# Kernel optimization log

Hardware: AMD Instinct MI355X
Metric: run time of the kernel (lower is better)

Reference implementation:

```python
import jax, jax.numpy as jnp
import numpy as np

N, D_IN, FC_DIM, GROUP, NONGT, EMB = 4096, 12544, 1024, 16, 300, 64
DG = FC_DIM // GROUP  # 64 per-head dim


def extract_position_matrix(bbox, nongt_dim):
    xmin, ymin, xmax, ymax = jnp.split(bbox, 4, axis=1)  # each [N,1]
    bw = xmax - xmin + 1.0
    bh = ymax - ymin + 1.0
    cx = 0.5 * (xmin + xmax)
    cy = 0.5 * (ymin + ymax)
    dx = jnp.log(jnp.maximum(jnp.abs((cx - cx.T) / bw), 1e-3))
    dy = jnp.log(jnp.maximum(jnp.abs((cy - cy.T) / bh), 1e-3))
    dw = jnp.log(bw / bw.T)
    dh = jnp.log(bh / bh.T)
    # slice to first nongt_dim columns, stack -> [N, nongt, 4]
    return jnp.stack([dx[:, :nongt_dim], dy[:, :nongt_dim],
                      dw[:, :nongt_dim], dh[:, :nongt_dim]], axis=2)


def extract_position_embedding(pos_mat, feat_dim=64, wave_length=1000.0):
    n8 = feat_dim // 8
    feat_range = jnp.arange(n8, dtype=pos_mat.dtype)
    dim_mat = wave_length ** (8.0 / feat_dim * feat_range)  # [8]
    div = 100.0 * pos_mat[..., None] / dim_mat              # [N,nongt,4,8]
    emb = jnp.concatenate([jnp.sin(div), jnp.cos(div)], axis=3)  # [N,nongt,4,16]
    return emb.reshape(pos_mat.shape[0], pos_mat.shape[1], feat_dim)


def attention_multi_head(feat, pos_emb, Wpos, bpos, Wq, bq, Wk, bk, Wo, bo):
    # feat: [N, 1024], pos_emb: [N, nongt, 64]
    nongt_feat = feat[:NONGT]                                   # [nongt, 1024]
    aff_w = jax.nn.relu(pos_emb @ Wpos + bpos)                  # [N, nongt, G]
    aff_w = jnp.swapaxes(aff_w, 1, 2)                           # [N, G, nongt]
    q = (feat @ Wq + bq).reshape(-1, GROUP, DG)                 # [N, G, dg]
    k = (nongt_feat @ Wk + bk).reshape(NONGT, GROUP, DG)        # [nongt, G, dg]
    aff = jnp.einsum('ngd,mgd->ngm', q, k) * (1.0 / np.sqrt(DG))  # [N, G, nongt]
    logits = jnp.log(jnp.maximum(aff_w, 1e-6)) + aff
    p = jax.nn.softmax(logits, axis=2)                          # [N, G, nongt]
    out = jnp.einsum('ngm,mc->ngc', p, nongt_feat)              # [N, G, 1024]
    # grouped 1x1 conv: group g maps 1024 -> 64 outputs
    lin = jnp.einsum('ngc,goc->ngo', out, Wo) + bo.reshape(GROUP, DG)
    return lin.reshape(feat.shape[0], FC_DIM)


def setup_inputs() -> dict:
    key = jax.random.key(0)
    ks = jax.random.split(key, 20)
    roi_feat = jax.random.normal(ks[0], (N, D_IN), dtype=jnp.float32)
    u = jax.random.uniform(ks[1], (N, 4), dtype=jnp.float32)
    x1 = u[:, 0:1] * 500.0
    y1 = u[:, 1:2] * 500.0
    bbox = jnp.concatenate([x1, y1, x1 + u[:, 2:3] * 200.0 + 1.0,
                            y1 + u[:, 3:4] * 200.0 + 1.0], axis=1)
    def lin(k, fin, fout):
        s = 1.0 / np.sqrt(fin)
        return jax.random.normal(k, (fin, fout), dtype=jnp.float32) * s
    inp = {'roi_feat': roi_feat, 'bbox': bbox,
           'W_fc1': lin(ks[2], D_IN, FC_DIM), 'b_fc1': jnp.zeros((FC_DIM,), jnp.float32),
           'W_fc2': lin(ks[3], FC_DIM, FC_DIM), 'b_fc2': jnp.zeros((FC_DIM,), jnp.float32)}
    for i, base in [(1, 4), (2, 10)]:
        inp[f'Wpos{i}'] = lin(ks[base], EMB, GROUP)
        inp[f'bpos{i}'] = jnp.zeros((GROUP,), jnp.float32)
        inp[f'Wq{i}'] = lin(ks[base + 1], FC_DIM, FC_DIM)
        inp[f'bq{i}'] = jnp.zeros((FC_DIM,), jnp.float32)
        inp[f'Wk{i}'] = lin(ks[base + 2], FC_DIM, FC_DIM)
        inp[f'bk{i}'] = jnp.zeros((FC_DIM,), jnp.float32)
        inp[f'Wo{i}'] = jax.random.normal(ks[base + 3], (GROUP, DG, FC_DIM), dtype=jnp.float32) * (1.0 / np.sqrt(FC_DIM))
        inp[f'bo{i}'] = jnp.zeros((FC_DIM,), jnp.float32)
    return inp


def reference(roi_feat, bbox, W_fc1, b_fc1, W_fc2, b_fc2,
              Wpos1, bpos1, Wq1, bq1, Wk1, bk1, Wo1, bo1,
              Wpos2, bpos2, Wq2, bq2, Wk2, bk2, Wo2, bo2):
    pos_mat = extract_position_matrix(bbox, NONGT)
    pos_emb = extract_position_embedding(pos_mat, EMB)
    x = roi_feat
    for (Wf, bf, Wp, bp, Wq, bq, Wk, bk, Wo, bo) in [
        (W_fc1, b_fc1, Wpos1, bpos1, Wq1, bq1, Wk1, bk1, Wo1, bo1),
        (W_fc2, b_fc2, Wpos2, bpos2, Wq2, bq2, Wk2, bk2, Wo2, bo2)]:
        x = x @ Wf + bf
        attn = attention_multi_head(x, pos_emb, Wp, bp, Wq, bq, Wk, bk, Wo, bo)
        x = jax.nn.relu(x + attn)
    return x
```

## Files before the change

kernel.cpp:

```cpp
#include <hip/hip_runtime.h>


using bf16x8 = __attribute__((ext_vector_type(8))) short;
using u16x4  = __attribute__((ext_vector_type(4))) short;
using f32x4  = __attribute__((ext_vector_type(4))) float;
typedef unsigned short u16;
typedef unsigned int   u32;

#define DEV __device__ __forceinline__

DEV u32 cvtpk(float lo, float hi) {
  u32 r;
  asm("v_cvt_pk_bf16_f32 %0, %1, %2" : "=v"(r) : "v"(lo), "v"(hi));
  return r;
}
DEV u16 f2bf(float f) { return (u16)cvtpk(f, f); }
DEV float bf2f(u16 h) { return __uint_as_float(((u32)h) << 16); }

DEV f32x4 mfma16(bf16x8 a, bf16x8 b, f32x4 c) {
  return __builtin_amdgcn_mfma_f32_16x16x32_bf16(a, b, c, 0, 0, 0);
}
DEV void gload16(const u16* g, u16* l) {
  __builtin_amdgcn_global_load_lds((const __attribute__((address_space(1))) void*)g,
                                   (__attribute__((address_space(3))) void*)l, 16, 0, 0);
}

DEV void fsincos(float x, float* s, float* c) {
  float r = x * 0.15915494309189535f;
  r -= rintf(r);
  float a = r * 6.283185307179586f;
  *s = __sinf(a); *c = __cosf(a);
}

struct PrepArgs {
  const float* Wo1; u16* Wo1_b;
  const float* Wo2; u16* Wo2_b;
  const float* Wfc1; u16* Wfc1_t;
  const float* wsrc[5]; u16* wdst[5];
};

__global__ __launch_bounds__(256) void prep_kernel(PrepArgs p) {
  __shared__ float tp[32][36];
  int b = blockIdx.x, tid = threadIdx.x;
  if (b < 1024) {
    const float* src = (b < 512) ? p.Wo1 : p.Wo2;
    u16* dst = (b < 512) ? p.Wo1_b : p.Wo2_b;
    size_t i = ((size_t)(b & 511) * 256 + tid) * 8;
    float4 a = *(const float4*)(src + i);
    float4 c = *(const float4*)(src + i + 4);
    int4 v;
    v.x = (int)cvtpk(a.x, a.y); v.y = (int)cvtpk(a.z, a.w);
    v.z = (int)cvtpk(c.x, c.y); v.w = (int)cvtpk(c.z, c.w);
    *(int4*)(dst + i) = v;
    return;
  }
  const float* in; u16* out; int r0, c0, R, C;
  if (b < 13568) {
    int idx = b - 1024;
    in = p.Wfc1; out = p.Wfc1_t; R = 12544; C = 1024;
    r0 = (idx >> 5) * 32; c0 = (idx & 31) * 32;
  } else {
    int idx = b - 13568;
    int z = idx >> 10, rest = idx & 1023;
    in = p.wsrc[z]; out = p.wdst[z]; R = 1024; C = 1024;
    r0 = (rest >> 5) * 32; c0 = (rest & 31) * 32;
  }
  {
    int r = tid >> 3, c4 = (tid & 7) * 4;
    float4 v = *(const float4*)(in + (size_t)(r0 + r) * C + c0 + c4);
    *(float4*)&tp[r][c4] = v;
  }
  __syncthreads();
  {
    int c = tid >> 3, r4 = (tid & 7) * 4;
    u32 lo = cvtpk(tp[r4 + 0][c], tp[r4 + 1][c]);
    u32 hi = cvtpk(tp[r4 + 2][c], tp[r4 + 3][c]);
    int2 v; v.x = (int)lo; v.y = (int)hi;
    *(int2*)(out + (size_t)(c0 + c) * R + r0 + r4) = v;
  }
}

__global__ __launch_bounds__(512, 2) void gemm8p(
    const float* __restrict__ A, const u16* __restrict__ Bt,
    float* __restrict__ P) {
  const int K = 12544;
  __shared__ u16 lds[65536];
  int tid = threadIdx.x;
  int w = tid >> 6, l = tid & 63, h = l >> 4, l15 = l & 15;
  int wm = w >> 2, wn = w & 3;

  int b = ((blockIdx.x & 7) << 5) | (blockIdx.x >> 3);
  int bz = b >> 6, rest = b & 63;
  int bm = (rest & 15) * 256;
  int bn = (rest >> 4) * 256;
  size_t k0 = (size_t)bz * 3136;

  int arow = tid >> 3;
  int c0 = (tid & 7) * 8;
  const float* pA0 = A + (size_t)(bm + arow) * K + k0 + c0;
  const size_t aseg = (size_t)64 * K;
  int awe = ((arow * 128 + c0 * 2) ^ ((arow & 7) << 4)) >> 1;

  int X = ((tid >> 3) & 7) << 4;
  int lb2 = (tid * 16) ^ X;
  int lr = lb2 >> 7, lc = (lb2 & 127) >> 1;
  const u16* pB = Bt + (size_t)(bn + lr) * K + k0 + lc;
  const size_t o64 = (size_t)64 * K, o128 = (size_t)128 * K, o192 = (size_t)192 * K;

  int swz = (l15 & 7) << 3;
  int xk0 = (h * 8) ^ swz;
  int xk1 = 32 ^ xk0;
  int rA = (wm * 64 + l15) * 64;
  int rB = (wn * 32 + l15) * 64;

  f32x4 acc[8][4];
#pragma unroll
  for (int i = 0; i < 8; i++)
#pragma unroll
    for (int j = 0; j < 4; j++) acc[i][j] = (f32x4){0.f, 0.f, 0.f, 0.f};

  float4 a0[4], a1[4];
  bf16x8 af[4][2], bl[2][2], bh[2][2];

#define AISSUE(kk) { _Pragma("unroll") for (int s = 0; s < 4; s++) {     \
    a0[s] = *(const float4*)(pA0 + s * aseg + (kk));                     \
    a1[s] = *(const float4*)(pA0 + s * aseg + (kk) + 4); } }
#define BISSUE_LO(WB, kk) {                                              \
    gload16(pB + (kk),        (WB) + tid * 8);                           \
    gload16(pB + o64 + (kk),  (WB) + 4096 + tid * 8); }
#define BISSUE_HI(WB, kk) {                                              \
    gload16(pB + o128 + (kk), (WB) + 8192 + tid * 8);                    \
    gload16(pB + o192 + (kk), (WB) + 12288 + tid * 8); }
#define AWRITE(WA) { _Pragma("unroll") for (int s = 0; s < 4; s++) {     \
    int4 v;                                                              \
    v.x = (int)cvtpk(a0[s].x, a0[s].y);                                  \
    v.y = (int)cvtpk(a0[s].z, a0[s].w);                                  \
    v.z = (int)cvtpk(a1[s].x, a1[s].y);                                  \
    v.w = (int)cvtpk(a1[s].z, a1[s].w);                                  \
    *(int4*)&(WA)[awe + s * 4096] = v; } }
#define READ_AF(BASE)                                                    \
  _Pragma("unroll") for (int i = 0; i < 4; i++) {                        \
    af[i][0] = *(const bf16x8*)&LA[(BASE) + rA + i * 1024 + xk0];        \
    af[i][1] = *(const bf16x8*)&LA[(BASE) + rA + i * 1024 + xk1];        \
  }
#define READ_BL {                                                        \
  _Pragma("unroll") for (int j = 0; j < 2; j++) {                        \
    bl[j][0] = *(const bf16x8*)&LB[rB + j * 1024 + xk0];                 \
    bl[j][1] = *(const bf16x8*)&LB[rB + j * 1024 + xk1]; } }
#define READ_BH {                                                        \
  _Pragma("unroll") for (int j = 0; j < 2; j++) {                        \
    bh[j][0] = *(const bf16x8*)&LB[8192 + rB + j * 1024 + xk0];          \
    bh[j][1] = *(const bf16x8*)&LB[8192 + rB + j * 1024 + xk1]; } }
#define Q_MFMA(QR, QC, BF)                                               \
  __builtin_amdgcn_s_setprio(1);                                         \
  _Pragma("unroll") for (int i = 0; i < 4; i++)                          \
    _Pragma("unroll") for (int j = 0; j < 2; j++) {                      \
      acc[(QR)*4+i][(QC)*2+j] = mfma16(af[i][0], BF[j][0], acc[(QR)*4+i][(QC)*2+j]); \
      acc[(QR)*4+i][(QC)*2+j] = mfma16(af[i][1], BF[j][1], acc[(QR)*4+i][(QC)*2+j]); \
    }                                                                    \
  __builtin_amdgcn_s_setprio(0);
#define SBAR __builtin_amdgcn_sched_barrier(0)

  AISSUE(0);
  BISSUE_LO(lds + 16384, 0);
  BISSUE_HI(lds + 16384, 0);
  AWRITE(lds);
  asm volatile("s_waitcnt vmcnt(0) lgkmcnt(0)" ::: "memory");
  __builtin_amdgcn_s_barrier();

  for (int t = 0; t < 48; t++) {
    const u16* LA = lds + (t & 1) * 32768;
    const u16* LB = LA + 16384;
    u16* WA = lds + ((t + 1) & 1) * 32768;
    u16* WB = WA + 16384;
    int ktn = (t + 1) * 64;
    AISSUE(ktn);
    asm volatile("s_waitcnt vmcnt(10) lgkmcnt(0)" ::: "memory");
    __builtin_amdgcn_s_barrier();
    SBAR;
    READ_AF(0);
    READ_BL;
    Q_MFMA(0, 0, bl);
    SBAR;
    BISSUE_LO(WB, ktn);
    asm volatile("s_waitcnt vmcnt(10)" ::: "memory");
    __builtin_amdgcn_s_barrier();
    SBAR;
    READ_BH;
    Q_MFMA(0, 1, bh);
    SBAR;
    BISSUE_HI(WB, ktn);
    READ_AF(8192);
    Q_MFMA(1, 1, bh);
    SBAR;
    Q_MFMA(1, 0, bl);
    SBAR;
    AWRITE(WA);
  }
  {
    const u16* LA = lds;
    const u16* LB = lds + 16384;
    asm volatile("s_waitcnt vmcnt(2) lgkmcnt(0)" ::: "memory");
    __builtin_amdgcn_s_barrier();
    SBAR;
    READ_AF(0);
    READ_BL;
    Q_MFMA(0, 0, bl);
    SBAR;
    asm volatile("s_waitcnt vmcnt(0)" ::: "memory");
    __builtin_amdgcn_s_barrier();
    SBAR;
    READ_BH;
    Q_MFMA(0, 1, bh);
    SBAR;
    READ_AF(8192);
    Q_MFMA(1, 1, bh);
    Q_MFMA(1, 0, bl);
  }
#undef AISSUE
#undef BISSUE_LO
#undef BISSUE_HI
#undef AWRITE
#undef READ_AF
#undef READ_BL
#undef READ_BH
#undef Q_MFMA
#undef SBAR

  float* dst = P + (size_t)bz * 4096 * 1024;
#pragma unroll
  for (int qr = 0; qr < 2; qr++)
#pragma unroll
    for (int i = 0; i < 4; i++)
#pragma unroll
      for (int qc = 0; qc < 2; qc++)
#pragma unroll
        for (int j = 0; j < 2; j++) {
          int row0 = bm + qr * 128 + wm * 64 + i * 16 + h * 4;
          int col  = bn + qc * 128 + wn * 32 + j * 16 + l15;
          f32x4 v = acc[qr * 4 + i][qc * 2 + j];
#pragma unroll
          for (int r = 0; r < 4; r++)
            dst[(size_t)(row0 + r) * 1024 + col] = v[r];
        }
}

__constant__ float C100D[8] = {100.f, 42.16965034285822f, 17.78279410038923f,
                               7.498942093324559f, 3.1622776601683795f,
                               1.333521432163324f, 0.5623413251903491f,
                               0.23713737056616552f};

__global__ __launch_bounds__(256) void reduce_pos_kernel(
    const float* __restrict__ P, const float* __restrict__ bias,
    float* __restrict__ xf, u16* __restrict__ xb,
    const float* __restrict__ bbox,
    const float* __restrict__ Wpos1, const float* __restrict__ Wpos2,
    const float* __restrict__ bpos1, const float* __restrict__ bpos2,
    u16* __restrict__ logw1, u16* __restrict__ logw2) {
  __shared__ u16 pool[18944];
  int tid = threadIdx.x;
  if (blockIdx.x < 2048) {
    const size_t MN = (size_t)4096 * 1024;
    size_t i = ((size_t)blockIdx.x * 256 + tid) * 4;
    size_t stride = (size_t)2048 * 256 * 4;
    for (; i < MN; i += stride) {
      float4 a = *(const float4*)(P + i);
      float4 b = *(const float4*)(P + MN + i);
      float4 c = *(const float4*)(P + 2 * MN + i);
      float4 d = *(const float4*)(P + 3 * MN + i);
      float4 bv = *(const float4*)(bias + (i & 1023));
      float4 r;
      r.x = a.x + b.x + c.x + d.x + bv.x;
      r.y = a.y + b.y + c.y + d.y + bv.y;
      r.z = a.z + b.z + c.z + d.z + bv.z;
      r.w = a.w + b.w + c.w + d.w + bv.w;
      *(float4*)(xf + i) = r;
      int2 hv; hv.x = (int)cvtpk(r.x, r.y); hv.y = (int)cvtpk(r.z, r.w);
      *(int2*)(xb + i) = hv;
    }
    return;
  }
  u16* emb_s = pool;
  u16* wp_s  = pool + 5632;
  u16* lw_s  = pool + 8448;
  int n = blockIdx.x - 2048;
  int w = tid >> 6, l = tid & 63, h = l >> 4, l15 = l & 15;
  for (int idx = tid; idx < 1024; idx += 256) {
    int e = idx >> 4, c = idx & 15;
    wp_s[c * 88 + e]        = f2bf(Wpos1[idx]);
    wp_s[(16 + c) * 88 + e] = f2bf(Wpos2[idx]);
  }
  float4 bn = ((const float4*)bbox)[n];
  float bw_n = bn.z - bn.x + 1.f, bh_n = bn.w - bn.y + 1.f;
  float cx_n = 0.5f * (bn.x + bn.z), cy_n = 0.5f * (bn.y + bn.w);
  float bps0 = bpos1[l15], bps1 = bpos2[l15];
  int p = tid >> 2, k = tid & 3;

  for (int m0 = 0; m0 < 320; m0 += 64) {
    int m = m0 + p;
    float4 bm = ((const float4*)bbox)[m];
    float v;
    if (k == 0)      v = logf(fmaxf(fabsf((cx_n - 0.5f * (bm.x + bm.z)) / bw_n), 1e-3f));
    else if (k == 1) v = logf(fmaxf(fabsf((cy_n - 0.5f * (bm.y + bm.w)) / bh_n), 1e-3f));
    else if (k == 2) v = logf(bw_n / (bm.z - bm.x + 1.f));
    else             v = logf(bh_n / (bm.w - bm.y + 1.f));
    __syncthreads();
#pragma unroll
    for (int tt = 0; tt < 8; tt++) {
      float s, c; fsincos(v * C100D[tt], &s, &c);
      emb_s[p * 88 + k * 16 + tt]     = f2bf(s);
      emb_s[p * 88 + k * 16 + 8 + tt] = f2bf(c);
    }
    __syncthreads();
    f32x4 acc0 = {0.f, 0.f, 0.f, 0.f}, acc1 = {0.f, 0.f, 0.f, 0.f};
    bf16x8 a0 = *(const bf16x8*)&emb_s[(w * 16 + l15) * 88 + h * 8];
    bf16x8 a1 = *(const bf16x8*)&emb_s[(w * 16 + l15) * 88 + 32 + h * 8];
    bf16x8 b00 = *(const bf16x8*)&wp_s[l15 * 88 + h * 8];
    bf16x8 b01 = *(const bf16x8*)&wp_s[l15 * 88 + 32 + h * 8];
    bf16x8 b10 = *(const bf16x8*)&wp_s[(16 + l15) * 88 + h * 8];
    bf16x8 b11 = *(const bf16x8*)&wp_s[(16 + l15) * 88 + 32 + h * 8];
    acc0 = mfma16(a0, b00, acc0); acc0 = mfma16(a1, b01, acc0);
    acc1 = mfma16(a0, b10, acc1); acc1 = mfma16(a1, b11, acc1);
#pragma unroll
    for (int r = 0; r < 4; r++) {
      int mm = m0 + w * 16 + h * 4 + r;
      lw_s[l15 * 328 + mm]        = f2bf(logf(fmaxf(acc0[r] + bps0, 1e-6f)));
      lw_s[(16 + l15) * 328 + mm] = f2bf(logf(fmaxf(acc1[r] + bps1, 1e-6f)));
    }
  }
  __syncthreads();
  for (int i = tid; i < 1280; i += 256) {
    int layer = i / 640, rest = i - layer * 640;
    int gg = rest / 40, seg = rest - gg * 40;
    bf16x8 v = *(const bf16x8*)&lw_s[(layer * 16 + gg) * 328 + seg * 8];
    u16* dst = (layer ? logw2 : logw1) + ((size_t)gg * 4096 + n) * 320 + seg * 8;
    *(bf16x8*)dst = v;
  }
}

struct GDesc {
  const u16* A; const u16* Bt; const float* bias;
  u16* Cb; float* Cf;
  int M, N, K, ldc, nt;
};

__global__ __launch_bounds__(256, 2) void gemmU(GDesc g0, GDesc g1, GDesc g2,
                                                int c0, int c1) {
  __shared__ u16 lds[32768];
  GDesc g; int lb = blockIdx.x;
  if (lb < c0) { g = g0; lb = (lb & 7) * (c0 >> 3) + (lb >> 3); }
  else if (lb < c1) { g = g1; lb -= c0; }
  else { g = g2; lb -= c1; }
  int bm = (lb / g.nt) * 128, bn = (lb % g.nt) * 128;
  int tid = threadIdx.x;
  int w = tid >> 6, l = tid & 63, h = l >> 4, l15 = l & 15;
  int wm = w >> 1, wn = w & 1;
  int K = g.K;

  int X = ((tid >> 3) & 7) << 4;
  int lbyte = (tid * 16) ^ X;
  int lr = lbyte >> 7, lc = (lbyte & 127) >> 1;
  const u16 *pa[4], *pb[4];
#pragma unroll
  for (int c = 0; c < 4; c++) {
    pa[c] = g.A  + (size_t)min(bm + c * 32 + lr, g.M - 1) * K + lc;
    pb[c] = g.Bt + (size_t)min(bn + c * 32 + lr, g.N - 1) * K + lc;
  }

  int swz = (l15 & 7) << 3;
  int xk0 = (h * 8) ^ swz;
  int xk1 = 32 ^ xk0;
  int rA = (wm * 64 + l15) * 64;
  int rB = (wn * 64 + l15) * 64;

  f32x4 acc[4][4];
#pragma unroll
  for (int i = 0; i < 4; i++)
#pragma unroll
    for (int j = 0; j < 4; j++) acc[i][j] = (f32x4){0.f, 0.f, 0.f, 0.f};

#define ISSUEU(W, kk)                                     \
  { gload16(pa[0] + (kk), (W) + tid * 8);                 \
    gload16(pa[1] + (kk), (W) + 2048 + tid * 8);          \
    gload16(pa[2] + (kk), (W) + 4096 + tid * 8);          \
    gload16(pa[3] + (kk), (W) + 6144 + tid * 8);          \
    gload16(pb[0] + (kk), (W) + 8192 + tid * 8);          \
    gload16(pb[1] + (kk), (W) + 10240 + tid * 8);         \
    gload16(pb[2] + (kk), (W) + 12288 + tid * 8);         \
    gload16(pb[3] + (kk), (W) + 14336 + tid * 8); }

  ISSUEU(lds, 0);
  int ktiles = K >> 6;
  for (int t = 0; t < ktiles; t++) {
    const u16* LA = lds + (t & 1) * 16384;
    const u16* LB = LA + 8192;
    u16* W = lds + ((t ^ 1) & 1) * 16384;
    if (t < ktiles - 1) {
      ISSUEU(W, (t + 1) * 64);
      asm volatile("s_waitcnt vmcnt(8)" ::: "memory");
    } else {
      asm volatile("s_waitcnt vmcnt(0)" ::: "memory");
    }
    __builtin_amdgcn_s_barrier();
    asm volatile("" ::: "memory");
    bf16x8 a[4][2], bfr[4][2];
#pragma unroll
    for (int i = 0; i < 4; i++) {
      a[i][0] = *(const bf16x8*)&LA[rA + i * 1024 + xk0];
      a[i][1] = *(const bf16x8*)&LA[rA + i * 1024 + xk1];
    }
#pragma unroll
    for (int j = 0; j < 4; j++) {
      bfr[j][0] = *(const bf16x8*)&LB[rB + j * 1024 + xk0];
      bfr[j][1] = *(const bf16x8*)&LB[rB + j * 1024 + xk1];
    }
    __builtin_amdgcn_s_setprio(1);
#pragma unroll
    for (int i = 0; i < 4; i++)
#pragma unroll
      for (int j = 0; j < 4; j++) {
        acc[i][j] = mfma16(a[i][0], bfr[j][0], acc[i][j]);
        acc[i][j] = mfma16(a[i][1], bfr[j][1], acc[i][j]);
      }
    __builtin_amdgcn_s_setprio(0);
    asm volatile("" ::: "memory");
    __builtin_amdgcn_s_barrier();
  }
#undef ISSUEU

#pragma unroll
  for (int i = 0; i < 4; i++) {
#pragma unroll
    for (int j = 0; j < 4; j++) {
      int col = bn + wn * 64 + j * 16 + l15;
      if (col >= g.ldc) continue;
      float bv = (g.bias != nullptr && col < g.N) ? g.bias[col] : 0.f;
      int row0 = bm + wm * 64 + i * 16 + h * 4;
#pragma unroll
      for (int r = 0; r < 4; r++) {
        int row = row0 + r;
        if (row >= g.M) continue;
        float v = acc[i][j][r] + bv;
        size_t off = (size_t)row * g.ldc + col;
        g.Cb[off] = f2bf(v);
        if (g.Cf != nullptr) g.Cf[off] = v;
      }
    }
  }
}

template <bool LAST>
__global__ __launch_bounds__(256) void attn_kernel(
    const u16* __restrict__ qb, const u16* __restrict__ kb,
    const u16* __restrict__ kvt, const u16* __restrict__ logw,
    const float* __restrict__ xf, const float* __restrict__ bo,
    float* __restrict__ outf, u16* __restrict__ outb) {
  __shared__ u16 ps[64 * 344];
  int tid = threadIdx.x;
  int g = blockIdx.y, n0 = blockIdx.x * 64;
  int w = tid >> 6, l = tid & 63, h = l >> 4, l15 = l & 15;

  {
    const u16* src = logw + ((size_t)g * 4096 + n0) * 320;
    for (int i = tid; i < 64 * 40; i += 256) {
      int row = i / 40, seg = i - row * 40;
      *(bf16x8*)&ps[row * 328 + seg * 8] = *(const bf16x8*)(src + row * 320 + seg * 8);
    }
  }
  int nrow = n0 + w * 16 + l15;
  const u16* qp = qb + (size_t)nrow * 1024 + g * 64;
  bf16x8 aq0 = *(const bf16x8*)(qp + h * 8);
  bf16x8 aq1 = *(const bf16x8*)(qp + 32 + h * 8);

  f32x4 acc[19];
#pragma unroll
  for (int f = 0; f < 19; f++) acc[f] = (f32x4){0.f, 0.f, 0.f, 0.f};
  const u16* kp = kb + g * 64 + h * 8;
#pragma unroll
  for (int f = 0; f < 19; f++) {
    bf16x8 b0 = *(const bf16x8*)(kp + (size_t)(f * 16 + l15) * 1024);
    bf16x8 b1 = *(const bf16x8*)(kp + (size_t)(f * 16 + l15) * 1024 + 32);
    acc[f] = mfma16(aq0, b0, acc[f]);
    acc[f] = mfma16(aq1, b1, acc[f]);
  }
  __syncthreads();

  int nbase = n0 + w * 16 + h * 4;
  int lrow = w * 16 + h * 4;
  float mx[4] = {-INFINITY, -INFINITY, -INFINITY, -INFINITY};
  float sm[4] = {0.f, 0.f, 0.f, 0.f};
#pragma unroll
  for (int f = 0; f < 19; f++) {
    int m = f * 16 + l15;
#pragma unroll
    for (int r = 0; r < 4; r++) {
      float lw = -INFINITY;
      if (m < 300) lw = bf2f(ps[(lrow + r) * 328 + m]);
      float lg = acc[f][r] * 0.125f + lw;
      acc[f][r] = lg;
      mx[r] = fmaxf(mx[r], lg);
    }
  }
#pragma unroll
  for (int d = 1; d < 16; d <<= 1)
#pragma unroll
    for (int r = 0; r < 4; r++) mx[r] = fmaxf(mx[r], __shfl_xor(mx[r], d));
#pragma unroll
  for (int f = 0; f < 19; f++)
#pragma unroll
    for (int r = 0; r < 4; r++) {
      float p = __expf(acc[f][r] - mx[r]);
      acc[f][r] = p; sm[r] += p;
    }
#pragma unroll
  for (int d = 1; d < 16; d <<= 1)
#pragma unroll
    for (int r = 0; r < 4; r++) sm[r] += __shfl_xor(sm[r], d);
  float inv[4];
#pragma unroll
  for (int r = 0; r < 4; r++) inv[r] = 1.f / sm[r];

  __syncthreads();
#pragma unroll
  for (int f = 0; f < 19; f++)
#pragma unroll
    for (int r = 0; r < 4; r++)
      ps[(lrow + r) * 344 + f * 16 + l15] = f2bf(acc[f][r]);
#pragma unroll
  for (int r = 0; r < 4; r++)
    ps[(lrow + r) * 344 + 304 + l15] = 0;

  f32x4 acc2[4];
#pragma unroll
  for (int fo = 0; fo < 4; fo++) acc2[fo] = (f32x4){0.f, 0.f, 0.f, 0.f};
  const u16* vp = kvt + (size_t)g * 64 * 320 + h * 8;
#pragma unroll
  for (int ks = 0; ks < 10; ks++) {
    bf16x8 ap = *(const bf16x8*)&ps[(w * 16 + l15) * 344 + ks * 32 + h * 8];
#pragma unroll
    for (int fo = 0; fo < 4; fo++) {
      bf16x8 bv = *(const bf16x8*)(vp + (size_t)(fo * 16 + l15) * 320 + ks * 32);
      acc2[fo] = mfma16(ap, bv, acc2[fo]);
    }
  }
#pragma unroll
  for (int fo = 0; fo < 4; fo++) {
    int col = g * 64 + fo * 16 + l15;
    float bov = bo[col];
#pragma unroll
    for (int r = 0; r < 4; r++) {
      int row = nbase + r;
      float v = xf[(size_t)row * 1024 + col] + acc2[fo][r] * inv[r] + bov;
      v = fmaxf(v, 0.f);
      if (LAST) outf[(size_t)row * 1024 + col] = v;
      else      outb[(size_t)row * 1024 + col] = f2bf(v);
    }
  }
}

extern "C" void kernel_launch(void* const* d_in, const int* in_sizes, int n_in,
                              void* d_out, int out_size, void* d_ws, size_t ws_size,
                              hipStream_t stream) {
  (void)in_sizes; (void)n_in; (void)out_size; (void)ws_size;
  const float* roi   = (const float*)d_in[0];
  const float* bbox  = (const float*)d_in[1];
  const float* Wfc1  = (const float*)d_in[2];
  const float* bfc1  = (const float*)d_in[3];
  const float* Wfc2  = (const float*)d_in[4];
  const float* bfc2  = (const float*)d_in[5];
  const float* Wpos1 = (const float*)d_in[6];
  const float* bpos1 = (const float*)d_in[7];
  const float* Wq1   = (const float*)d_in[8];
  const float* bq1   = (const float*)d_in[9];
  const float* Wk1   = (const float*)d_in[10];
  const float* bk1   = (const float*)d_in[11];
  const float* Wo1   = (const float*)d_in[12];
  const float* bo1   = (const float*)d_in[13];
  const float* Wpos2 = (const float*)d_in[14];
  const float* bpos2 = (const float*)d_in[15];
  const float* Wq2   = (const float*)d_in[16];
  const float* bq2   = (const float*)d_in[17];
  const float* Wk2   = (const float*)d_in[18];
  const float* bk2   = (const float*)d_in[19];
  const float* Wo2   = (const float*)d_in[20];
  const float* bo2   = (const float*)d_in[21];

  char* ws = (char*)d_ws;
  u16*  Wfc1_t = (u16*)(ws + 102760448);
  u16*  Wfc2_t = (u16*)(ws + 128450560);
  u16*  Wq1_t  = (u16*)(ws + 130547712);
  u16*  Wk1_t  = (u16*)(ws + 132644864);
  u16*  Wq2_t  = (u16*)(ws + 134742016);
  u16*  Wk2_t  = (u16*)(ws + 136839168);
  u16*  Wo1_b  = (u16*)(ws + 138936320);
  u16*  Wo2_b  = (u16*)(ws + 141033472);
  float* Pp    = (float*)(ws + 143134720);
  float* xf    = (float*)(ws + 227020800);
  u16*  xb_f   = (u16*)(ws + 243798016);
  u16*  xb_a   = (u16*)(ws + 252186624);
  u16*  q_b    = (u16*)(ws + 260575232);
  u16*  k_b    = (u16*)(ws + 268963840);
  u16*  kvt_b  = (u16*)(ws + 269578240);
  u16*  logw1  = (u16*)(ws + 270233600);
  u16*  logw2  = (u16*)(ws + 312176640);

  {
    PrepArgs p;
    p.Wo1 = Wo1;   p.Wo1_b = Wo1_b;
    p.Wo2 = Wo2;   p.Wo2_b = Wo2_b;
    p.Wfc1 = Wfc1; p.Wfc1_t = Wfc1_t;
    p.wsrc[0] = Wfc2; p.wdst[0] = Wfc2_t;
    p.wsrc[1] = Wq1;  p.wdst[1] = Wq1_t;
    p.wsrc[2] = Wk1;  p.wdst[2] = Wk1_t;
    p.wsrc[3] = Wq2;  p.wdst[3] = Wq2_t;
    p.wsrc[4] = Wk2;  p.wdst[4] = Wk2_t;
    prep_kernel<<<18688, 256, 0, stream>>>(p);
  }
  gemm8p<<<256, 512, 0, stream>>>(roi, Wfc1_t, Pp);
  reduce_pos_kernel<<<6144, 256, 0, stream>>>(Pp, bfc1, xf, xb_f, bbox,
                                              Wpos1, Wpos2, bpos1, bpos2,
                                              logw1, logw2);
  {
    GDesc q  = {xb_f,  Wq1_t, bq1, q_b,   nullptr, 4096, 1024, 1024, 1024, 8};
    GDesc kk = {xb_f,  Wk1_t, bk1, k_b,   nullptr,  300, 1024, 1024, 1024, 8};
    GDesc kv = {Wo1_b, xb_f,  nullptr, kvt_b, nullptr, 1024, 300, 1024, 320, 3};
    gemmU<<<304, 256, 0, stream>>>(q, kk, kv, 256, 280);
  }
  attn_kernel<false><<<dim3(64, 16), 256, 0, stream>>>(q_b, k_b, kvt_b, logw1, xf, bo1, nullptr, xb_a);

  {
    GDesc fc = {xb_a, Wfc2_t, bfc2, xb_f, xf, 4096, 1024, 1024, 1024, 8};
    gemmU<<<256, 256, 0, stream>>>(fc, fc, fc, 256, 256);
  }
  {
    GDesc q  = {xb_f,  Wq2_t, bq2, q_b,   nullptr, 4096, 1024, 1024, 1024, 8};
    GDesc kk = {xb_f,  Wk2_t, bk2, k_b,   nullptr,  300, 1024, 1024, 1024, 8};
    GDesc kv = {Wo2_b, xb_f,  nullptr, kvt_b, nullptr, 1024, 300, 1024, 320, 3};
    gemmU<<<304, 256, 0, stream>>>(q, kk, kv, 256, 280);
  }
  attn_kernel<true><<<dim3(64, 16), 256, 0, stream>>>(q_b, k_b, kvt_b, logw2, xf, bo2, (float*)d_out, nullptr);
}
```

Baseline: 381.8 us.

## Move position-embedding work into prep kernel, drop fp32 residual copy, raise MFMA priority

The position-embedding and log-weight computation moves out of the post-GEMM reduce kernel and into the weight-prep kernel, so it no longer follows the big FC1 GEMM. The fp32 residual buffer xf is removed: the reduce and FC2 GEMM write only bf16, and the attention kernel reads the bf16 residual. This cuts fp32 write and read traffic. s_setprio is also placed around the MFMA loops in the attention kernel. The residual now carries bf16 rounding, which may reduce accuracy.

```diff
diff --git a/kernel.cpp b/kernel.cpp
--- a/kernel.cpp
+++ b/kernel.cpp
@@ -2,7 +2,6 @@
 
 
 using bf16x8 = __attribute__((ext_vector_type(8))) short;
-using u16x4  = __attribute__((ext_vector_type(4))) short;
 using f32x4  = __attribute__((ext_vector_type(4))) float;
 typedef unsigned short u16;
 typedef unsigned int   u32;
@@ -32,20 +31,89 @@
   *s = __sinf(a); *c = __cosf(a);
 }
 
-struct PrepArgs {
+__constant__ float C100D[8] = {100.f, 42.16965034285822f, 17.78279410038923f,
+                               7.498942093324559f, 3.1622776601683795f,
+                               1.333521432163324f, 0.5623413251903491f,
+                               0.23713737056616552f};
+
+struct PrepPosArgs {
+  const float* bbox;
+  const float* Wpos1; const float* Wpos2;
+  const float* bpos1; const float* bpos2;
+  u16* logw1; u16* logw2;
   const float* Wo1; u16* Wo1_b;
   const float* Wo2; u16* Wo2_b;
   const float* Wfc1; u16* Wfc1_t;
   const float* wsrc[5]; u16* wdst[5];
 };
 
-__global__ __launch_bounds__(256) void prep_kernel(PrepArgs p) {
-  __shared__ float tp[32][36];
+__global__ __launch_bounds__(256) void prep_pos_kernel(PrepPosArgs p) {
+  __shared__ u16 pool[18944];
   int b = blockIdx.x, tid = threadIdx.x;
-  if (b < 1024) {
-    const float* src = (b < 512) ? p.Wo1 : p.Wo2;
-    u16* dst = (b < 512) ? p.Wo1_b : p.Wo2_b;
-    size_t i = ((size_t)(b & 511) * 256 + tid) * 8;
+  if (b < 4096) {
+    u16* emb_s = pool;
+    u16* wp_s  = pool + 5632;
+    u16* lw_s  = pool + 8448;
+    int n = b;
+    int w = tid >> 6, l = tid & 63, h = l >> 4, l15 = l & 15;
+    for (int idx = tid; idx < 1024; idx += 256) {
+      int e = idx >> 4, c = idx & 15;
+      wp_s[c * 88 + e]        = f2bf(p.Wpos1[idx]);
+      wp_s[(16 + c) * 88 + e] = f2bf(p.Wpos2[idx]);
+    }
+    float4 bn = ((const float4*)p.bbox)[n];
+    float bw_n = bn.z - bn.x + 1.f, bh_n = bn.w - bn.y + 1.f;
+    float cx_n = 0.5f * (bn.x + bn.z), cy_n = 0.5f * (bn.y + bn.w);
+    float bps0 = p.bpos1[l15], bps1 = p.bpos2[l15];
+    int pr = tid >> 2, k = tid & 3;
+
+    for (int m0 = 0; m0 < 320; m0 += 64) {
+      int m = m0 + pr;
+      float4 bm = ((const float4*)p.bbox)[m];
+      float v;
+      if (k == 0)      v = logf(fmaxf(fabsf((cx_n - 0.5f * (bm.x + bm.z)) / bw_n), 1e-3f));
+      else if (k == 1) v = logf(fmaxf(fabsf((cy_n - 0.5f * (bm.y + bm.w)) / bh_n), 1e-3f));
+      else if (k == 2) v = logf(bw_n / (bm.z - bm.x + 1.f));
+      else             v = logf(bh_n / (bm.w - bm.y + 1.f));
+      __syncthreads();
+#pragma unroll
+      for (int tt = 0; tt < 8; tt++) {
+        float s, c; fsincos(v * C100D[tt], &s, &c);
+        emb_s[pr * 88 + k * 16 + tt]     = f2bf(s);
+        emb_s[pr * 88 + k * 16 + 8 + tt] = f2bf(c);
+      }
+      __syncthreads();
+      f32x4 acc0 = {0.f, 0.f, 0.f, 0.f}, acc1 = {0.f, 0.f, 0.f, 0.f};
+      bf16x8 a0 = *(const bf16x8*)&emb_s[(w * 16 + l15) * 88 + h * 8];
+      bf16x8 a1 = *(const bf16x8*)&emb_s[(w * 16 + l15) * 88 + 32 + h * 8];
+      bf16x8 b00 = *(const bf16x8*)&wp_s[l15 * 88 + h * 8];
+      bf16x8 b01 = *(const bf16x8*)&wp_s[l15 * 88 + 32 + h * 8];
+      bf16x8 b10 = *(const bf16x8*)&wp_s[(16 + l15) * 88 + h * 8];
+      bf16x8 b11 = *(const bf16x8*)&wp_s[(16 + l15) * 88 + 32 + h * 8];
+      acc0 = mfma16(a0, b00, acc0); acc0 = mfma16(a1, b01, acc0);
+      acc1 = mfma16(a0, b10, acc1); acc1 = mfma16(a1, b11, acc1);
+#pragma unroll
+      for (int r = 0; r < 4; r++) {
+        int mm = m0 + w * 16 + h * 4 + r;
+        lw_s[l15 * 328 + mm]        = f2bf(logf(fmaxf(acc0[r] + bps0, 1e-6f)));
+        lw_s[(16 + l15) * 328 + mm] = f2bf(logf(fmaxf(acc1[r] + bps1, 1e-6f)));
+      }
+    }
+    __syncthreads();
+    for (int i = tid; i < 1280; i += 256) {
+      int layer = i / 640, rest = i - layer * 640;
+      int gg = rest / 40, seg = rest - gg * 40;
+      bf16x8 v = *(const bf16x8*)&lw_s[(layer * 16 + gg) * 328 + seg * 8];
+      u16* dst = (layer ? p.logw2 : p.logw1) + ((size_t)gg * 4096 + n) * 320 + seg * 8;
+      *(bf16x8*)dst = v;
+    }
+    return;
+  }
+  int b2 = b - 4096;
+  if (b2 < 1024) {
+    const float* src = (b2 < 512) ? p.Wo1 : p.Wo2;
+    u16* dst = (b2 < 512) ? p.Wo1_b : p.Wo2_b;
+    size_t i = ((size_t)(b2 & 511) * 256 + tid) * 8;
     float4 a = *(const float4*)(src + i);
     float4 c = *(const float4*)(src + i + 4);
     int4 v;
@@ -54,13 +122,14 @@
     *(int4*)(dst + i) = v;
     return;
   }
+  float (*tp)[36] = (float(*)[36])pool;
   const float* in; u16* out; int r0, c0, R, C;
-  if (b < 13568) {
-    int idx = b - 1024;
+  if (b2 < 13568) {
+    int idx = b2 - 1024;
     in = p.Wfc1; out = p.Wfc1_t; R = 12544; C = 1024;
     r0 = (idx >> 5) * 32; c0 = (idx & 31) * 32;
   } else {
-    int idx = b - 13568;
+    int idx = b2 - 13568;
     int z = idx >> 10, rest = idx & 1023;
     in = p.wsrc[z]; out = p.wdst[z]; R = 1024; C = 1024;
     r0 = (rest >> 5) * 32; c0 = (rest & 31) * 32;
@@ -73,9 +142,9 @@
   __syncthreads();
   {
     int c = tid >> 3, r4 = (tid & 7) * 4;
-    u32 lo = cvtpk(tp[r4 + 0][c], tp[r4 + 1][c]);
-    u32 hi = cvtpk(tp[r4 + 2][c], tp[r4 + 3][c]);
-    int2 v; v.x = (int)lo; v.y = (int)hi;
+    int2 v;
+    v.x = (int)cvtpk(tp[r4 + 0][c], tp[r4 + 1][c]);
+    v.y = (int)cvtpk(tp[r4 + 2][c], tp[r4 + 3][c]);
     *(int2*)(out + (size_t)(c0 + c) * R + r0 + r4) = v;
   }
 }
@@ -245,102 +314,31 @@
         }
 }
 
-__constant__ float C100D[8] = {100.f, 42.16965034285822f, 17.78279410038923f,
-                               7.498942093324559f, 3.1622776601683795f,
-                               1.333521432163324f, 0.5623413251903491f,
-                               0.23713737056616552f};
-
-__global__ __launch_bounds__(256) void reduce_pos_kernel(
+__global__ __launch_bounds__(256) void reduce_kernel(
     const float* __restrict__ P, const float* __restrict__ bias,
-    float* __restrict__ xf, u16* __restrict__ xb,
-    const float* __restrict__ bbox,
-    const float* __restrict__ Wpos1, const float* __restrict__ Wpos2,
-    const float* __restrict__ bpos1, const float* __restrict__ bpos2,
-    u16* __restrict__ logw1, u16* __restrict__ logw2) {
-  __shared__ u16 pool[18944];
-  int tid = threadIdx.x;
-  if (blockIdx.x < 2048) {
-    const size_t MN = (size_t)4096 * 1024;
-    size_t i = ((size_t)blockIdx.x * 256 + tid) * 4;
-    size_t stride = (size_t)2048 * 256 * 4;
-    for (; i < MN; i += stride) {
-      float4 a = *(const float4*)(P + i);
-      float4 b = *(const float4*)(P + MN + i);
-      float4 c = *(const float4*)(P + 2 * MN + i);
-      float4 d = *(const float4*)(P + 3 * MN + i);
-      float4 bv = *(const float4*)(bias + (i & 1023));
-      float4 r;
-      r.x = a.x + b.x + c.x + d.x + bv.x;
-      r.y = a.y + b.y + c.y + d.y + bv.y;
-      r.z = a.z + b.z + c.z + d.z + bv.z;
-      r.w = a.w + b.w + c.w + d.w + bv.w;
-      *(float4*)(xf + i) = r;
-      int2 hv; hv.x = (int)cvtpk(r.x, r.y); hv.y = (int)cvtpk(r.z, r.w);
-      *(int2*)(xb + i) = hv;
-    }
-    return;
-  }
-  u16* emb_s = pool;
-  u16* wp_s  = pool + 5632;
-  u16* lw_s  = pool + 8448;
-  int n = blockIdx.x - 2048;
-  int w = tid >> 6, l = tid & 63, h = l >> 4, l15 = l & 15;
-  for (int idx = tid; idx < 1024; idx += 256) {
-    int e = idx >> 4, c = idx & 15;
-    wp_s[c * 88 + e]        = f2bf(Wpos1[idx]);
-    wp_s[(16 + c) * 88 + e] = f2bf(Wpos2[idx]);
-  }
-  float4 bn = ((const float4*)bbox)[n];
-  float bw_n = bn.z - bn.x + 1.f, bh_n = bn.w - bn.y + 1.f;
-  float cx_n = 0.5f * (bn.x + bn.z), cy_n = 0.5f * (bn.y + bn.w);
-  float bps0 = bpos1[l15], bps1 = bpos2[l15];
-  int p = tid >> 2, k = tid & 3;
-
-  for (int m0 = 0; m0 < 320; m0 += 64) {
-    int m = m0 + p;
-    float4 bm = ((const float4*)bbox)[m];
-    float v;
-    if (k == 0)      v = logf(fmaxf(fabsf((cx_n - 0.5f * (bm.x + bm.z)) / bw_n), 1e-3f));
-    else if (k == 1) v = logf(fmaxf(fabsf((cy_n - 0.5f * (bm.y + bm.w)) / bh_n), 1e-3f));
-    else if (k == 2) v = logf(bw_n / (bm.z - bm.x + 1.f));
-    else             v = logf(bh_n / (bm.w - bm.y + 1.f));
-    __syncthreads();
-#pragma unroll
-    for (int tt = 0; tt < 8; tt++) {
-      float s, c; fsincos(v * C100D[tt], &s, &c);
-      emb_s[p * 88 + k * 16 + tt]     = f2bf(s);
-      emb_s[p * 88 + k * 16 + 8 + tt] = f2bf(c);
-    }
-    __syncthreads();
-    f32x4 acc0 = {0.f, 0.f, 0.f, 0.f}, acc1 = {0.f, 0.f, 0.f, 0.f};
-    bf16x8 a0 = *(const bf16x8*)&emb_s[(w * 16 + l15) * 88 + h * 8];
-    bf16x8 a1 = *(const bf16x8*)&emb_s[(w * 16 + l15) * 88 + 32 + h * 8];
-    bf16x8 b00 = *(const bf16x8*)&wp_s[l15 * 88 + h * 8];
-    bf16x8 b01 = *(const bf16x8*)&wp_s[l15 * 88 + 32 + h * 8];
-    bf16x8 b10 = *(const bf16x8*)&wp_s[(16 + l15) * 88 + h * 8];
-    bf16x8 b11 = *(const bf16x8*)&wp_s[(16 + l15) * 88 + 32 + h * 8];
-    acc0 = mfma16(a0, b00, acc0); acc0 = mfma16(a1, b01, acc0);
-    acc1 = mfma16(a0, b10, acc1); acc1 = mfma16(a1, b11, acc1);
-#pragma unroll
-    for (int r = 0; r < 4; r++) {
-      int mm = m0 + w * 16 + h * 4 + r;
-      lw_s[l15 * 328 + mm]        = f2bf(logf(fmaxf(acc0[r] + bps0, 1e-6f)));
-      lw_s[(16 + l15) * 328 + mm] = f2bf(logf(fmaxf(acc1[r] + bps1, 1e-6f)));
-    }
-  }
-  __syncthreads();
-  for (int i = tid; i < 1280; i += 256) {
-    int layer = i / 640, rest = i - layer * 640;
-    int gg = rest / 40, seg = rest - gg * 40;
-    bf16x8 v = *(const bf16x8*)&lw_s[(layer * 16 + gg) * 328 + seg * 8];
-    u16* dst = (layer ? logw2 : logw1) + ((size_t)gg * 4096 + n) * 320 + seg * 8;
-    *(bf16x8*)dst = v;
+    u16* __restrict__ xb) {
+  const size_t MN = (size_t)4096 * 1024;
+  size_t i = ((size_t)blockIdx.x * 256 + threadIdx.x) * 4;
+  size_t stride = (size_t)2048 * 256 * 4;
+  for (; i < MN; i += stride) {
+    float4 a = *(const float4*)(P + i);
+    float4 b = *(const float4*)(P + MN + i);
+    float4 c = *(const float4*)(P + 2 * MN + i);
+    float4 d = *(const float4*)(P + 3 * MN + i);
+    float4 bv = *(const float4*)(bias + (i & 1023));
+    float4 r;
+    r.x = a.x + b.x + c.x + d.x + bv.x;
+    r.y = a.y + b.y + c.y + d.y + bv.y;
+    r.z = a.z + b.z + c.z + d.z + bv.z;
+    r.w = a.w + b.w + c.w + d.w + bv.w;
+    int2 hv; hv.x = (int)cvtpk(r.x, r.y); hv.y = (int)cvtpk(r.z, r.w);
+    *(int2*)(xb + i) = hv;
   }
 }
 
 struct GDesc {
   const u16* A; const u16* Bt; const float* bias;
-  u16* Cb; float* Cf;
+  u16* Cb;
   int M, N, K, ldc, nt;
 };
 
@@ -440,10 +438,7 @@
       for (int r = 0; r < 4; r++) {
         int row = row0 + r;
         if (row >= g.M) continue;
-        float v = acc[i][j][r] + bv;
-        size_t off = (size_t)row * g.ldc + col;
-        g.Cb[off] = f2bf(v);
-        if (g.Cf != nullptr) g.Cf[off] = v;
+        g.Cb[(size_t)row * g.ldc + col] = f2bf(acc[i][j][r] + bv);
       }
     }
   }
@@ -453,7 +448,7 @@
 __global__ __launch_bounds__(256) void attn_kernel(
     const u16* __restrict__ qb, const u16* __restrict__ kb,
     const u16* __restrict__ kvt, const u16* __restrict__ logw,
-    const float* __restrict__ xf, const float* __restrict__ bo,
+    const u16* __restrict__ xr, const float* __restrict__ bo,
     float* __restrict__ outf, u16* __restrict__ outb) {
   __shared__ u16 ps[64 * 344];
   int tid = threadIdx.x;
@@ -476,6 +471,7 @@
 #pragma unroll
   for (int f = 0; f < 19; f++) acc[f] = (f32x4){0.f, 0.f, 0.f, 0.f};
   const u16* kp = kb + g * 64 + h * 8;
+  __builtin_amdgcn_s_setprio(1);
 #pragma unroll
   for (int f = 0; f < 19; f++) {
     bf16x8 b0 = *(const bf16x8*)(kp + (size_t)(f * 16 + l15) * 1024);
@@ -483,6 +479,7 @@
     acc[f] = mfma16(aq0, b0, acc[f]);
     acc[f] = mfma16(aq1, b1, acc[f]);
   }
+  __builtin_amdgcn_s_setprio(0);
   __syncthreads();
 
   int nbase = n0 + w * 16 + h * 4;
@@ -534,6 +531,7 @@
 #pragma unroll
   for (int fo = 0; fo < 4; fo++) acc2[fo] = (f32x4){0.f, 0.f, 0.f, 0.f};
   const u16* vp = kvt + (size_t)g * 64 * 320 + h * 8;
+  __builtin_amdgcn_s_setprio(1);
 #pragma unroll
   for (int ks = 0; ks < 10; ks++) {
     bf16x8 ap = *(const bf16x8*)&ps[(w * 16 + l15) * 344 + ks * 32 + h * 8];
@@ -543,6 +541,7 @@
       acc2[fo] = mfma16(ap, bv, acc2[fo]);
     }
   }
+  __builtin_amdgcn_s_setprio(0);
 #pragma unroll
   for (int fo = 0; fo < 4; fo++) {
     int col = g * 64 + fo * 16 + l15;
@@ -550,10 +549,11 @@
 #pragma unroll
     for (int r = 0; r < 4; r++) {
       int row = nbase + r;
-      float v = xf[(size_t)row * 1024 + col] + acc2[fo][r] * inv[r] + bov;
+      size_t off = (size_t)row * 1024 + col;
+      float v = bf2f(xr[off]) + acc2[fo][r] * inv[r] + bov;
       v = fmaxf(v, 0.f);
-      if (LAST) outf[(size_t)row * 1024 + col] = v;
-      else      outb[(size_t)row * 1024 + col] = f2bf(v);
+      if (LAST) outf[off] = v;
+      else      outb[off] = f2bf(v);
     }
   }
 }
@@ -595,7 +595,6 @@
   u16*  Wo1_b  = (u16*)(ws + 138936320);
   u16*  Wo2_b  = (u16*)(ws + 141033472);
   float* Pp    = (float*)(ws + 143134720);
-  float* xf    = (float*)(ws + 227020800);
   u16*  xb_f   = (u16*)(ws + 243798016);
   u16*  xb_a   = (u16*)(ws + 252186624);
   u16*  q_b    = (u16*)(ws + 260575232);
@@ -605,7 +604,11 @@
   u16*  logw2  = (u16*)(ws + 312176640);
 
   {
-    PrepArgs p;
+    PrepPosArgs p;
+    p.bbox = bbox;
+    p.Wpos1 = Wpos1; p.Wpos2 = Wpos2;
+    p.bpos1 = bpos1; p.bpos2 = bpos2;
+    p.logw1 = logw1; p.logw2 = logw2;
     p.Wo1 = Wo1;   p.Wo1_b = Wo1_b;
     p.Wo2 = Wo2;   p.Wo2_b = Wo2_b;
     p.Wfc1 = Wfc1; p.Wfc1_t = Wfc1_t;
@@ -614,29 +617,27 @@
     p.wsrc[2] = Wk1;  p.wdst[2] = Wk1_t;
     p.wsrc[3] = Wq2;  p.wdst[3] = Wq2_t;
     p.wsrc[4] = Wk2;  p.wdst[4] = Wk2_t;
-    prep_kernel<<<18688, 256, 0, stream>>>(p);
+    prep_pos_kernel<<<22784, 256, 0, stream>>>(p);
   }
   gemm8p<<<256, 512, 0, stream>>>(roi, Wfc1_t, Pp);
-  reduce_pos_kernel<<<6144, 256, 0, stream>>>(Pp, bfc1, xf, xb_f, bbox,
-                                              Wpos1, Wpos2, bpos1, bpos2,
-                                              logw1, logw2);
-  {
-    GDesc q  = {xb_f,  Wq1_t, bq1, q_b,   nullptr, 4096, 1024, 1024, 1024, 8};
-    GDesc kk = {xb_f,  Wk1_t, bk1, k_b,   nullptr,  300, 1024, 1024, 1024, 8};
-    GDesc kv = {Wo1_b, xb_f,  nullptr, kvt_b, nullptr, 1024, 300, 1024, 320, 3};
+  reduce_kernel<<<2048, 256, 0, stream>>>(Pp, bfc1, xb_f);
+  {
+    GDesc q  = {xb_f,  Wq1_t, bq1, q_b,   4096, 1024, 1024, 1024, 8};
+    GDesc kk = {xb_f,  Wk1_t, bk1, k_b,    300, 1024, 1024, 1024, 8};
+    GDesc kv = {Wo1_b, xb_f,  nullptr, kvt_b, 1024, 300, 1024, 320, 3};
     gemmU<<<304, 256, 0, stream>>>(q, kk, kv, 256, 280);
   }
-  attn_kernel<false><<<dim3(64, 16), 256, 0, stream>>>(q_b, k_b, kvt_b, logw1, xf, bo1, nullptr, xb_a);
-
-  {
-    GDesc fc = {xb_a, Wfc2_t, bfc2, xb_f, xf, 4096, 1024, 1024, 1024, 8};
+  attn_kernel<false><<<dim3(64, 16), 256, 0, stream>>>(q_b, k_b, kvt_b, logw1, xb_f, bo1, nullptr, xb_a);
+
+  {
+    GDesc fc = {xb_a, Wfc2_t, bfc2, xb_f, 4096, 1024, 1024, 1024, 8};
     gemmU<<<256, 256, 0, stream>>>(fc, fc, fc, 256, 256);
   }
   {
-    GDesc q  = {xb_f,  Wq2_t, bq2, q_b,   nullptr, 4096, 1024, 1024, 1024, 8};
-    GDesc kk = {xb_f,  Wk2_t, bk2, k_b,   nullptr,  300, 1024, 1024, 1024, 8};
-    GDesc kv = {Wo2_b, xb_f,  nullptr, kvt_b, nullptr, 1024, 300, 1024, 320, 3};
+    GDesc q  = {xb_f,  Wq2_t, bq2, q_b,   4096, 1024, 1024, 1024, 8};
+    GDesc kk = {xb_f,  Wk2_t, bk2, k_b,    300, 1024, 1024, 1024, 8};
+    GDesc kv = {Wo2_b, xb_f,  nullptr, kvt_b, 1024, 300, 1024, 320, 3};
     gemmU<<<304, 256, 0, stream>>>(q, kk, kv, 256, 280);
   }
-  attn_kernel<true><<<dim3(64, 16), 256, 0, stream>>>(q_b, k_b, kvt_b, logw2, xf, bo2, (float*)d_out, nullptr);
-}
+  attn_kernel<true><<<dim3(64, 16), 256, 0, stream>>>(q_b, k_b, kvt_b, logw2, xb_f, bo2, (float*)d_out, nullptr);
+}
```

Result: slower. 405.4 us (+6.2%).
